# Kernel tuning notes

Hardware: AMD Instinct MI355X
Metric: run time of the kernel (lower is better)

The kernel has to match this reference:

```python
import jax, jax.numpy as jnp
import numpy as np

NUM_ITERATIONS = 3


def squash(t, axis=-1):
    # scale * t / sqrt(||t||^2), scale = ||t||^2 / (1 + ||t||^2)
    sq = jnp.sum(t * t, axis=axis, keepdims=True)
    return (sq / (1.0 + sq)) * t / jnp.sqrt(sq)


def setup_inputs() -> dict:
    key = jax.random.key(0)
    k1, k2 = jax.random.split(key)
    x = jax.random.normal(k1, (256, 1152, 8), dtype=jnp.float32)
    route_weights = jax.random.normal(k2, (10, 1152, 8, 16), dtype=jnp.float32)
    return {"x": x, "route_weights": route_weights}


def reference(x, route_weights):
    # priors[c,b,n,1,o] = x[b,n,:] @ route_weights[c,n,:,:]
    priors = jnp.einsum('bni,cnio->cbno', x, route_weights)[:, :, :, None, :]
    logits = jnp.zeros_like(priors)
    outputs = None
    for i in range(NUM_ITERATIONS):
        probs = jax.nn.softmax(logits, axis=2)  # softmax over route nodes (dim=2), as in source
        outputs = squash(jnp.sum(probs * priors, axis=2, keepdims=True))  # [c,b,1,1,o]
        if i != NUM_ITERATIONS - 1:
            delta = jnp.sum(priors * outputs, axis=-1, keepdims=True)  # [c,b,n,1,1]
            logits = logits + delta  # broadcasts over last dim
    return outputs
```

## Files before the change

### kernel.cpp

```cpp
#include <hip/hip_runtime.h>

#define NCAP 10
#define NB   256
#define NN   1152
#define KI   8
#define NO   16
#define NT   1024
#define NWV  16
#define TB   2
#define NITER 3

typedef float v2f __attribute__((ext_vector_type(2)));

__global__ __launch_bounds__(NT, 8) void capsule_kernel(
    const float* __restrict__ x,
    const float* __restrict__ w,
    float* __restrict__ out)
{
    __shared__ unsigned s_pr[TB * NN * 8];
    __shared__ float s_red2[NWV][TB][NO];
    __shared__ float s_ls[NWV][TB];
    __shared__ float s_v[TB][NO];

    const int t    = threadIdx.x;
    const int wv   = t >> 6;
    const int lane = t & 63;
    const int j    = t & 3;
    const int g    = t >> 2;

    const int bid = blockIdx.x;
    const int swz = (bid & 7) * (NCAP * (NB / TB) / 8) + (bid >> 3);
    const int c   = swz / (NB / TB);
    const int b0  = (swz % (NB / TB)) * TB;

    const int bl0 = lane & 1, bl1 = (lane >> 1) & 1,
              bl2 = (lane >> 2) & 1, bl3 = (lane >> 3) & 1;

    auto slotof = [](int n, int q) { return 2 * n + (q ^ ((n >> 2) & 1)); };

    float bs[TB][4] = {{0.f,0.f,0.f,0.f},{0.f,0.f,0.f,0.f}};

    auto build_round = [&](int n) {
        const float4* wp = reinterpret_cast<const float4*>(
            w + ((size_t)c * NN + n) * (KI * NO));
        float xs[TB][KI];
        #pragma unroll
        for (int tb = 0; tb < TB; ++tb) {
            const float4* xp = reinterpret_cast<const float4*>(
                x + ((size_t)(b0 + tb) * NN + n) * KI);
            float4 a = xp[0], b = xp[1];
            xs[tb][0]=a.x; xs[tb][1]=a.y; xs[tb][2]=a.z; xs[tb][3]=a.w;
            xs[tb][4]=b.x; xs[tb][5]=b.y; xs[tb][6]=b.z; xs[tb][7]=b.w;
        }
        float acc[TB][4] = {{0.f,0.f,0.f,0.f},{0.f,0.f,0.f,0.f}};
        #pragma unroll
        for (int i = 0; i < KI; ++i) {
            float4 wq = wp[i * 4 + j];
            #pragma unroll
            for (int tb = 0; tb < TB; ++tb) {
                acc[tb][0] = fmaf(xs[tb][i], wq.x, acc[tb][0]);
                acc[tb][1] = fmaf(xs[tb][i], wq.y, acc[tb][1]);
                acc[tb][2] = fmaf(xs[tb][i], wq.z, acc[tb][2]);
                acc[tb][3] = fmaf(xs[tb][i], wq.w, acc[tb][3]);
            }
        }
        const int q = j >> 1, h = j & 1;
        #pragma unroll
        for (int tb = 0; tb < TB; ++tb) {
            bs[tb][0] += acc[tb][0]; bs[tb][1] += acc[tb][1];
            bs[tb][2] += acc[tb][2]; bs[tb][3] += acc[tb][3];
            unsigned p0, p1;
            asm("v_cvt_pk_bf16_f32 %0, %1, %2"
                : "=v"(p0) : "v"(acc[tb][0]), "v"(acc[tb][1]));
            asm("v_cvt_pk_bf16_f32 %0, %1, %2"
                : "=v"(p1) : "v"(acc[tb][2]), "v"(acc[tb][3]));
            uint2 pk; pk.x = p0; pk.y = p1;
            *reinterpret_cast<uint2*>(
                &s_pr[tb * (NN * 8) + slotof(n, q) * 4 + h * 2]) = pk;
        }
    };
    #pragma unroll 1
    for (int r = 0; r < 4; ++r) build_round(r * 256 + g);
    if (g < 128) build_round(1024 + g);

    #pragma unroll
    for (int tb = 0; tb < TB; ++tb)
        #pragma unroll
        for (int k = 0; k < 4; ++k) {
            float s = bs[tb][k];
            s += __shfl_xor(s, 4);  s += __shfl_xor(s, 8);
            s += __shfl_xor(s, 16); s += __shfl_xor(s, 32);
            bs[tb][k] = s;
        }
    if (lane < 4) {
        #pragma unroll
        for (int tb = 0; tb < TB; ++tb) {
            s_red2[wv][tb][4*lane+0] = bs[tb][0];
            s_red2[wv][tb][4*lane+1] = bs[tb][1];
            s_red2[wv][tb][4*lane+2] = bs[tb][2];
            s_red2[wv][tb][4*lane+3] = bs[tb][3];
        }
    }
    __syncthreads();

    auto finalize = [&](int iter) {
        if (t < TB * NO) {
            const int tb = t >> 4, oc = t & 15;
            float acc = 0.f, lt = 0.f;
            #pragma unroll
            for (int w2 = 0; w2 < NWV; ++w2) {
                acc += s_red2[w2][tb][oc];
                if (iter > 0) lt += s_ls[w2][tb];
            }
            if (iter == 0) lt = (float)NN;
            float s_o = acc / lt;
            float sq = s_o * s_o;
            sq += __shfl_xor(sq, 1); sq += __shfl_xor(sq, 2);
            sq += __shfl_xor(sq, 4); sq += __shfl_xor(sq, 8);
            float scale = sq / ((1.f + sq) * sqrtf(sq));
            float vo = s_o * scale;
            s_v[tb][oc] = vo;
            if (iter == NITER - 1)
                out[((size_t)c * NB + b0 + tb) * NO + oc] = vo;
        }
    };

    float logit[2][TB] = {{0.f,0.f},{0.f,0.f}};

    auto routing_pass = [&]() {
        #pragma unroll
        for (int tb = 0; tb < TB; ++tb) {
            v2f vv2[8];
            {
                const float4* vp = reinterpret_cast<const float4*>(&s_v[tb][0]);
                float4 a = vp[0], b = vp[1], cc = vp[2], d4 = vp[3];
                vv2[0] = v2f{a.x,  a.y};  vv2[1] = v2f{a.z,  a.w};
                vv2[2] = v2f{b.x,  b.y};  vv2[3] = v2f{b.z,  b.w};
                vv2[4] = v2f{cc.x, cc.y}; vv2[5] = v2f{cc.z, cc.w};
                vv2[6] = v2f{d4.x, d4.y}; vv2[7] = v2f{d4.z, d4.w};
            }
            v2f sp2[8];
            #pragma unroll
            for (int p = 0; p < 8; ++p) sp2[p] = v2f{0.f, 0.f};
            float lse = 0.f;
            #pragma unroll
            for (int rr = 0; rr < 2; ++rr) {
                if (rr == 1 && t >= 128) continue;
                const int n = rr * 1024 + t;
                const unsigned* base = &s_pr[tb * (NN * 8)];
                uint4 qa = *reinterpret_cast<const uint4*>(&base[slotof(n, 0) * 4]);
                uint4 qb = *reinterpret_cast<const uint4*>(&base[slotof(n, 1) * 4]);
                unsigned u[8] = {qa.x, qa.y, qa.z, qa.w, qb.x, qb.y, qb.z, qb.w};
                v2f r2[8];
                #pragma unroll
                for (int op = 0; op < 8; ++op) {
                    r2[op].x = __uint_as_float(u[op] << 16);
                    r2[op].y = __uint_as_float(u[op] & 0xffff0000u);
                }
                v2f d2 = v2f{0.f, 0.f};
                #pragma unroll
                for (int op = 0; op < 8; ++op)
                    d2 = __builtin_elementwise_fma(r2[op], vv2[op], d2);
                logit[rr][tb] += d2.x + d2.y;
                float e = __expf(logit[rr][tb]);
                lse += e;
                v2f e2 = v2f{e, e};
                #pragma unroll
                for (int op = 0; op < 8; ++op)
                    sp2[op] = __builtin_elementwise_fma(e2, r2[op], sp2[op]);
            }
            float s = lse;
            s += __shfl_xor(s, 1);  s += __shfl_xor(s, 2);
            s += __shfl_xor(s, 4);  s += __shfl_xor(s, 8);
            s += __shfl_xor(s, 16); s += __shfl_xor(s, 32);
            if (lane == 0) s_ls[wv][tb] = s;
            float g8[8];
            #pragma unroll
            for (int r = 0; r < 8; ++r) {
                float keep = bl0 ? sp2[r].y : sp2[r].x;
                float send = bl0 ? sp2[r].x : sp2[r].y;
                g8[r] = keep + __shfl_xor(send, 1);
            }
            float g4[4];
            #pragma unroll
            for (int r = 0; r < 4; ++r) {
                float keep = bl1 ? g8[2*r+1] : g8[2*r];
                float send = bl1 ? g8[2*r]   : g8[2*r+1];
                g4[r] = keep + __shfl_xor(send, 2);
            }
            float g2[2];
            #pragma unroll
            for (int r = 0; r < 2; ++r) {
                float keep = bl2 ? g4[2*r+1] : g4[2*r];
                float send = bl2 ? g4[2*r]   : g4[2*r+1];
                g2[r] = keep + __shfl_xor(send, 4);
            }
            float g1;
            {
                float keep = bl3 ? g2[1] : g2[0];
                float send = bl3 ? g2[0] : g2[1];
                g1 = keep + __shfl_xor(send, 8);
            }
            g1 += __shfl_xor(g1, 16);
            g1 += __shfl_xor(g1, 32);
            if (lane < NO) s_red2[wv][tb][lane] = g1;
        }
    };

    finalize(0);
    __syncthreads();
    routing_pass();
    __syncthreads();
    finalize(1);
    __syncthreads();
    routing_pass();
    __syncthreads();
    finalize(2);
}

extern "C" void kernel_launch(void* const* d_in, const int* in_sizes, int n_in,
                              void* d_out, int out_size, void* d_ws, size_t ws_size,
                              hipStream_t stream) {
    const float* x = (const float*)d_in[0];
    const float* w = (const float*)d_in[1];
    float* out = (float*)d_out;
    capsule_kernel<<<dim3(NCAP * (NB / TB)), dim3(NT), 0, stream>>>(x, w, out);
}
```

Before: 62.66 us.

## Convert to persistent warp-specialized kernel overlapping prior build with routing

Launches 256 persistent blocks that each process 5 problems in sequence. The first half of the threads build the bf16 priors for the next problem into a double-buffered LDS array. At the same time, the second half runs the routing iterations on the previous problem. This is meant to hide global-load latency of the build phase behind routing compute and to remove the idle serial phases of the old one-block-per-problem design. The cost is twice the LDS use, fewer waves per phase, and a barrier-coupled schedule where the slower half sets the pace.

```diff
diff --git a/kernel.cpp b/kernel.cpp
--- a/kernel.cpp
+++ b/kernel.cpp
@@ -6,216 +6,229 @@
 #define KI   8
 #define NO   16
 #define NT   1024
-#define NWV  16
 #define TB   2
-#define NITER 3
+#define NPROB 5
+#define NBLK 256
 
 typedef float v2f __attribute__((ext_vector_type(2)));
 
-__global__ __launch_bounds__(NT, 8) void capsule_kernel(
+__global__ __launch_bounds__(NT, 4) void capsule_kernel(
     const float* __restrict__ x,
     const float* __restrict__ w,
     float* __restrict__ out)
 {
-    __shared__ unsigned s_pr[TB * NN * 8];
-    __shared__ float s_red2[NWV][TB][NO];
-    __shared__ float s_ls[NWV][TB];
-    __shared__ float s_v[TB][NO];
-
-    const int t    = threadIdx.x;
-    const int wv   = t >> 6;
-    const int lane = t & 63;
-    const int j    = t & 3;
-    const int g    = t >> 2;
-
-    const int bid = blockIdx.x;
-    const int swz = (bid & 7) * (NCAP * (NB / TB) / 8) + (bid >> 3);
-    const int c   = swz / (NB / TB);
-    const int b0  = (swz % (NB / TB)) * TB;
-
+    __shared__ unsigned s_pr[2][TB * NN * 8];
+    __shared__ float s_bsw[8][TB][NO];
+    __shared__ float s_rp[2][8][TB][NO];
+    __shared__ float s_lse[2][8][TB];
+
+    const int t = threadIdx.x, wv = t >> 6, lane = t & 63, bid = blockIdx.x;
+    const int j = t & 3, g2 = t >> 2;
+    const int rt = t - 512, rwv = wv - 8;
+    const int tb2 = (lane >> 4) & 1, oc = lane & 15;
     const int bl0 = lane & 1, bl1 = (lane >> 1) & 1,
-              bl2 = (lane >> 2) & 1, bl3 = (lane >> 3) & 1;
+              bl2v = (lane >> 2) & 1, bl3 = (lane >> 3) & 1;
 
     auto slotof = [](int n, int q) { return 2 * n + (q ^ ((n >> 2) & 1)); };
-
-    float bs[TB][4] = {{0.f,0.f,0.f,0.f},{0.f,0.f,0.f,0.f}};
-
-    auto build_round = [&](int n) {
-        const float4* wp = reinterpret_cast<const float4*>(
-            w + ((size_t)c * NN + n) * (KI * NO));
-        float xs[TB][KI];
-        #pragma unroll
-        for (int tb = 0; tb < TB; ++tb) {
-            const float4* xp = reinterpret_cast<const float4*>(
-                x + ((size_t)(b0 + tb) * NN + n) * KI);
-            float4 a = xp[0], b = xp[1];
-            xs[tb][0]=a.x; xs[tb][1]=a.y; xs[tb][2]=a.z; xs[tb][3]=a.w;
-            xs[tb][4]=b.x; xs[tb][5]=b.y; xs[tb][6]=b.z; xs[tb][7]=b.w;
+    auto squash = [&](float s_o) {
+        float sq = s_o * s_o;
+        sq += __shfl_xor(sq, 1); sq += __shfl_xor(sq, 2);
+        sq += __shfl_xor(sq, 4); sq += __shfl_xor(sq, 8);
+        return s_o * (sq / ((1.f + sq) * sqrtf(sq)));
+    };
+
+    #pragma unroll 1
+    for (int k = 0; k <= NPROB; ++k) {
+        const int parB = k & 1, parR = parB ^ 1;
+        const bool do_build = (k < NPROB), do_route = (k >= 1);
+        const int Pb = k * NBLK + bid;
+        const int swzB = (Pb & 7) * 160 + (Pb >> 3);
+        const int cB = swzB >> 7, b0B = (swzB & 127) * 2;
+        const int Pr = (k - 1) * NBLK + bid;
+        const int swzR = (Pr & 7) * 160 + (Pr >> 3);
+        const int cR = swzR >> 7, b0R = (swzR & 127) * 2;
+
+        float bs[TB][4] = {{0.f,0.f,0.f,0.f},{0.f,0.f,0.f,0.f}};
+        float logit[3][TB];
+        float vo = 0.f;
+
+        auto build_round = [&](int n) {
+            const float4* wp = reinterpret_cast<const float4*>(
+                w + ((size_t)cB * NN + n) * (KI * NO));
+            float xs[TB][KI];
+            #pragma unroll
+            for (int tb = 0; tb < TB; ++tb) {
+                const float4* xp = reinterpret_cast<const float4*>(
+                    x + ((size_t)(b0B + tb) * NN + n) * KI);
+                float4 a = xp[0], b = xp[1];
+                xs[tb][0]=a.x; xs[tb][1]=a.y; xs[tb][2]=a.z; xs[tb][3]=a.w;
+                xs[tb][4]=b.x; xs[tb][5]=b.y; xs[tb][6]=b.z; xs[tb][7]=b.w;
+            }
+            float4 wq[KI];
+            #pragma unroll
+            for (int i = 0; i < KI; ++i) wq[i] = wp[i * 4 + j];
+            float acc[TB][4] = {{0.f,0.f,0.f,0.f},{0.f,0.f,0.f,0.f}};
+            #pragma unroll
+            for (int i = 0; i < KI; ++i)
+                #pragma unroll
+                for (int tb = 0; tb < TB; ++tb) {
+                    acc[tb][0] = fmaf(xs[tb][i], wq[i].x, acc[tb][0]);
+                    acc[tb][1] = fmaf(xs[tb][i], wq[i].y, acc[tb][1]);
+                    acc[tb][2] = fmaf(xs[tb][i], wq[i].z, acc[tb][2]);
+                    acc[tb][3] = fmaf(xs[tb][i], wq[i].w, acc[tb][3]);
+                }
+            const int q = j >> 1, h = j & 1;
+            #pragma unroll
+            for (int tb = 0; tb < TB; ++tb) {
+                bs[tb][0] += acc[tb][0]; bs[tb][1] += acc[tb][1];
+                bs[tb][2] += acc[tb][2]; bs[tb][3] += acc[tb][3];
+                unsigned p0, p1;
+                asm("v_cvt_pk_bf16_f32 %0, %1, %2"
+                    : "=v"(p0) : "v"(acc[tb][0]), "v"(acc[tb][1]));
+                asm("v_cvt_pk_bf16_f32 %0, %1, %2"
+                    : "=v"(p1) : "v"(acc[tb][2]), "v"(acc[tb][3]));
+                uint2 pk2; pk2.x = p0; pk2.y = p1;
+                *reinterpret_cast<uint2*>(
+                    &s_pr[parB][tb * (NN*8) + slotof(n, q) * 4 + h * 2]) = pk2;
+            }
+        };
+
+        auto route_iter = [&](bool first, int wpar) {
+            #pragma unroll
+            for (int tb = 0; tb < TB; ++tb) {
+                v2f vv2[8];
+                #pragma unroll
+                for (int o2 = 0; o2 < 8; ++o2) {
+                    vv2[o2].x = __shfl(vo, tb * 16 + 2 * o2);
+                    vv2[o2].y = __shfl(vo, tb * 16 + 2 * o2 + 1);
+                }
+                v2f sp2[8];
+                #pragma unroll
+                for (int p = 0; p < 8; ++p) sp2[p] = v2f{0.f, 0.f};
+                float lse = 0.f;
+                #pragma unroll
+                for (int row = 0; row < 3; ++row) {
+                    if (row < 2 || rt < 128) {
+                        const int n = row * 512 + rt;
+                        const unsigned* base = &s_pr[parR][tb * (NN * 8)];
+                        uint4 qa = *reinterpret_cast<const uint4*>(&base[slotof(n, 0) * 4]);
+                        uint4 qb = *reinterpret_cast<const uint4*>(&base[slotof(n, 1) * 4]);
+                        unsigned u[8] = {qa.x, qa.y, qa.z, qa.w, qb.x, qb.y, qb.z, qb.w};
+                        v2f r2[8];
+                        #pragma unroll
+                        for (int op = 0; op < 8; ++op) {
+                            r2[op].x = __uint_as_float(u[op] << 16);
+                            r2[op].y = __uint_as_float(u[op] & 0xffff0000u);
+                        }
+                        v2f d2 = v2f{0.f, 0.f};
+                        #pragma unroll
+                        for (int op = 0; op < 8; ++op)
+                            d2 = __builtin_elementwise_fma(r2[op], vv2[op], d2);
+                        float lg = d2.x + d2.y;
+                        if (!first) lg += logit[row][tb];
+                        logit[row][tb] = lg;
+                        float e = __expf(lg);
+                        lse += e;
+                        v2f e2 = v2f{e, e};
+                        #pragma unroll
+                        for (int op = 0; op < 8; ++op)
+                            sp2[op] = __builtin_elementwise_fma(e2, r2[op], sp2[op]);
+                    }
+                }
+                float s = lse;
+                s += __shfl_xor(s, 1);  s += __shfl_xor(s, 2);
+                s += __shfl_xor(s, 4);  s += __shfl_xor(s, 8);
+                s += __shfl_xor(s, 16); s += __shfl_xor(s, 32);
+                if (lane == 0) s_lse[wpar][rwv][tb] = s;
+                float g8[8];
+                #pragma unroll
+                for (int r = 0; r < 8; ++r) {
+                    float keep = bl0 ? sp2[r].y : sp2[r].x;
+                    float send = bl0 ? sp2[r].x : sp2[r].y;
+                    g8[r] = keep + __shfl_xor(send, 1);
+                }
+                float g4[4];
+                #pragma unroll
+                for (int r = 0; r < 4; ++r) {
+                    float keep = bl1 ? g8[2*r+1] : g8[2*r];
+                    float send = bl1 ? g8[2*r]   : g8[2*r+1];
+                    g4[r] = keep + __shfl_xor(send, 2);
+                }
+                float g2x[2];
+                #pragma unroll
+                for (int r = 0; r < 2; ++r) {
+                    float keep = bl2v ? g4[2*r+1] : g4[2*r];
+                    float send = bl2v ? g4[2*r]   : g4[2*r+1];
+                    g2x[r] = keep + __shfl_xor(send, 4);
+                }
+                float g1;
+                {
+                    float keep = bl3 ? g2x[1] : g2x[0];
+                    float send = bl3 ? g2x[0] : g2x[1];
+                    g1 = keep + __shfl_xor(send, 8);
+                }
+                g1 += __shfl_xor(g1, 16);
+                g1 += __shfl_xor(g1, 32);
+                if (lane < NO) s_rp[wpar][rwv][tb][lane] = g1;
+            }
+        };
+
+        if (t < 512) {
+            if (do_build) { build_round(g2); build_round(128 + g2); build_round(256 + g2); }
+        } else if (do_route) {
+            float acc = 0.f;
+            #pragma unroll
+            for (int w2 = 0; w2 < 8; ++w2) acc += s_bsw[w2][tb2][oc];
+            vo = squash(acc / (float)NN);
+            route_iter(true, 1);
         }
-        float acc[TB][4] = {{0.f,0.f,0.f,0.f},{0.f,0.f,0.f,0.f}};
-        #pragma unroll
-        for (int i = 0; i < KI; ++i) {
-            float4 wq = wp[i * 4 + j];
-            #pragma unroll
-            for (int tb = 0; tb < TB; ++tb) {
-                acc[tb][0] = fmaf(xs[tb][i], wq.x, acc[tb][0]);
-                acc[tb][1] = fmaf(xs[tb][i], wq.y, acc[tb][1]);
-                acc[tb][2] = fmaf(xs[tb][i], wq.z, acc[tb][2]);
-                acc[tb][3] = fmaf(xs[tb][i], wq.w, acc[tb][3]);
-            }
+        __syncthreads();
+        if (t < 512) {
+            if (do_build) { build_round(384 + g2); build_round(512 + g2); build_round(640 + g2); }
+        } else if (do_route) {
+            float acc = 0.f, lt = 0.f;
+            #pragma unroll
+            for (int w2 = 0; w2 < 8; ++w2) {
+                acc += s_rp[1][w2][tb2][oc]; lt += s_lse[1][w2][tb2];
+            }
+            vo = squash(acc / lt);
+            route_iter(false, 0);
         }
-        const int q = j >> 1, h = j & 1;
-        #pragma unroll
-        for (int tb = 0; tb < TB; ++tb) {
-            bs[tb][0] += acc[tb][0]; bs[tb][1] += acc[tb][1];
-            bs[tb][2] += acc[tb][2]; bs[tb][3] += acc[tb][3];
-            unsigned p0, p1;
-            asm("v_cvt_pk_bf16_f32 %0, %1, %2"
-                : "=v"(p0) : "v"(acc[tb][0]), "v"(acc[tb][1]));
-            asm("v_cvt_pk_bf16_f32 %0, %1, %2"
-                : "=v"(p1) : "v"(acc[tb][2]), "v"(acc[tb][3]));
-            uint2 pk; pk.x = p0; pk.y = p1;
-            *reinterpret_cast<uint2*>(
-                &s_pr[tb * (NN * 8) + slotof(n, q) * 4 + h * 2]) = pk;
+        __syncthreads();
+        if (t < 512) {
+            if (do_build) {
+                build_round(768 + g2); build_round(896 + g2); build_round(1024 + g2);
+                #pragma unroll
+                for (int tb = 0; tb < TB; ++tb)
+                    #pragma unroll
+                    for (int kk = 0; kk < 4; ++kk) {
+                        float s = bs[tb][kk];
+                        s += __shfl_xor(s, 4);  s += __shfl_xor(s, 8);
+                        s += __shfl_xor(s, 16); s += __shfl_xor(s, 32);
+                        bs[tb][kk] = s;
+                    }
+                if (lane < 4) {
+                    #pragma unroll
+                    for (int tb = 0; tb < TB; ++tb) {
+                        s_bsw[wv][tb][4*lane+0] = bs[tb][0];
+                        s_bsw[wv][tb][4*lane+1] = bs[tb][1];
+                        s_bsw[wv][tb][4*lane+2] = bs[tb][2];
+                        s_bsw[wv][tb][4*lane+3] = bs[tb][3];
+                    }
+                }
+            }
+        } else if (do_route) {
+            float acc = 0.f, lt = 0.f;
+            #pragma unroll
+            for (int w2 = 0; w2 < 8; ++w2) {
+                acc += s_rp[0][w2][tb2][oc]; lt += s_lse[0][w2][tb2];
+            }
+            vo = squash(acc / lt);
+            if (wv == 8 && lane < 32)
+                out[((size_t)cR * NB + b0R + tb2) * NO + oc] = vo;
         }
-    };
-    #pragma unroll 1
-    for (int r = 0; r < 4; ++r) build_round(r * 256 + g);
-    if (g < 128) build_round(1024 + g);
-
-    #pragma unroll
-    for (int tb = 0; tb < TB; ++tb)
-        #pragma unroll
-        for (int k = 0; k < 4; ++k) {
-            float s = bs[tb][k];
-            s += __shfl_xor(s, 4);  s += __shfl_xor(s, 8);
-            s += __shfl_xor(s, 16); s += __shfl_xor(s, 32);
-            bs[tb][k] = s;
-        }
-    if (lane < 4) {
-        #pragma unroll
-        for (int tb = 0; tb < TB; ++tb) {
-            s_red2[wv][tb][4*lane+0] = bs[tb][0];
-            s_red2[wv][tb][4*lane+1] = bs[tb][1];
-            s_red2[wv][tb][4*lane+2] = bs[tb][2];
-            s_red2[wv][tb][4*lane+3] = bs[tb][3];
-        }
+        __syncthreads();
     }
-    __syncthreads();
-
-    auto finalize = [&](int iter) {
-        if (t < TB * NO) {
-            const int tb = t >> 4, oc = t & 15;
-            float acc = 0.f, lt = 0.f;
-            #pragma unroll
-            for (int w2 = 0; w2 < NWV; ++w2) {
-                acc += s_red2[w2][tb][oc];
-                if (iter > 0) lt += s_ls[w2][tb];
-            }
-            if (iter == 0) lt = (float)NN;
-            float s_o = acc / lt;
-            float sq = s_o * s_o;
-            sq += __shfl_xor(sq, 1); sq += __shfl_xor(sq, 2);
-            sq += __shfl_xor(sq, 4); sq += __shfl_xor(sq, 8);
-            float scale = sq / ((1.f + sq) * sqrtf(sq));
-            float vo = s_o * scale;
-            s_v[tb][oc] = vo;
-            if (iter == NITER - 1)
-                out[((size_t)c * NB + b0 + tb) * NO + oc] = vo;
-        }
-    };
-
-    float logit[2][TB] = {{0.f,0.f},{0.f,0.f}};
-
-    auto routing_pass = [&]() {
-        #pragma unroll
-        for (int tb = 0; tb < TB; ++tb) {
-            v2f vv2[8];
-            {
-                const float4* vp = reinterpret_cast<const float4*>(&s_v[tb][0]);
-                float4 a = vp[0], b = vp[1], cc = vp[2], d4 = vp[3];
-                vv2[0] = v2f{a.x,  a.y};  vv2[1] = v2f{a.z,  a.w};
-                vv2[2] = v2f{b.x,  b.y};  vv2[3] = v2f{b.z,  b.w};
-                vv2[4] = v2f{cc.x, cc.y}; vv2[5] = v2f{cc.z, cc.w};
-                vv2[6] = v2f{d4.x, d4.y}; vv2[7] = v2f{d4.z, d4.w};
-            }
-            v2f sp2[8];
-            #pragma unroll
-            for (int p = 0; p < 8; ++p) sp2[p] = v2f{0.f, 0.f};
-            float lse = 0.f;
-            #pragma unroll
-            for (int rr = 0; rr < 2; ++rr) {
-                if (rr == 1 && t >= 128) continue;
-                const int n = rr * 1024 + t;
-                const unsigned* base = &s_pr[tb * (NN * 8)];
-                uint4 qa = *reinterpret_cast<const uint4*>(&base[slotof(n, 0) * 4]);
-                uint4 qb = *reinterpret_cast<const uint4*>(&base[slotof(n, 1) * 4]);
-                unsigned u[8] = {qa.x, qa.y, qa.z, qa.w, qb.x, qb.y, qb.z, qb.w};
-                v2f r2[8];
-                #pragma unroll
-                for (int op = 0; op < 8; ++op) {
-                    r2[op].x = __uint_as_float(u[op] << 16);
-                    r2[op].y = __uint_as_float(u[op] & 0xffff0000u);
-                }
-                v2f d2 = v2f{0.f, 0.f};
-                #pragma unroll
-                for (int op = 0; op < 8; ++op)
-                    d2 = __builtin_elementwise_fma(r2[op], vv2[op], d2);
-                logit[rr][tb] += d2.x + d2.y;
-                float e = __expf(logit[rr][tb]);
-                lse += e;
-                v2f e2 = v2f{e, e};
-                #pragma unroll
-                for (int op = 0; op < 8; ++op)
-                    sp2[op] = __builtin_elementwise_fma(e2, r2[op], sp2[op]);
-            }
-            float s = lse;
-            s += __shfl_xor(s, 1);  s += __shfl_xor(s, 2);
-            s += __shfl_xor(s, 4);  s += __shfl_xor(s, 8);
-            s += __shfl_xor(s, 16); s += __shfl_xor(s, 32);
-            if (lane == 0) s_ls[wv][tb] = s;
-            float g8[8];
-            #pragma unroll
-            for (int r = 0; r < 8; ++r) {
-                float keep = bl0 ? sp2[r].y : sp2[r].x;
-                float send = bl0 ? sp2[r].x : sp2[r].y;
-                g8[r] = keep + __shfl_xor(send, 1);
-            }
-            float g4[4];
-            #pragma unroll
-            for (int r = 0; r < 4; ++r) {
-                float keep = bl1 ? g8[2*r+1] : g8[2*r];
-                float send = bl1 ? g8[2*r]   : g8[2*r+1];
-                g4[r] = keep + __shfl_xor(send, 2);
-            }
-            float g2[2];
-            #pragma unroll
-            for (int r = 0; r < 2; ++r) {
-                float keep = bl2 ? g4[2*r+1] : g4[2*r];
-                float send = bl2 ? g4[2*r]   : g4[2*r+1];
-                g2[r] = keep + __shfl_xor(send, 4);
-            }
-            float g1;
-            {
-                float keep = bl3 ? g2[1] : g2[0];
-                float send = bl3 ? g2[0] : g2[1];
-                g1 = keep + __shfl_xor(send, 8);
-            }
-            g1 += __shfl_xor(g1, 16);
-            g1 += __shfl_xor(g1, 32);
-            if (lane < NO) s_red2[wv][tb][lane] = g1;
-        }
-    };
-
-    finalize(0);
-    __syncthreads();
-    routing_pass();
-    __syncthreads();
-    finalize(1);
-    __syncthreads();
-    routing_pass();
-    __syncthreads();
-    finalize(2);
 }
 
 extern "C" void kernel_launch(void* const* d_in, const int* in_sizes, int n_in,
@@ -224,5 +237,5 @@
     const float* x = (const float*)d_in[0];
     const float* w = (const float*)d_in[1];
     float* out = (float*)d_out;
-    capsule_kernel<<<dim3(NCAP * (NB / TB)), dim3(NT), 0, stream>>>(x, w, out);
+    capsule_kernel<<<dim3(NBLK), dim3(NT), 0, stream>>>(x, w, out);
 }
```

Result: faster. 57.64 us (-8.0%).
